# Performance work log

Measured on AMD Instinct MI355X. Metric: run time of the kernel, lower is better.

## Reference

```python
import jax, jax.numpy as jnp
import numpy as np

TD = 256  # text_dim


def conv1x1(x, w, b):
    # 1x1 conv == per-pixel matmul over channels; w: [out,in], x: [B,C,H,W]
    return jnp.einsum('oc,bchw->bohw', w, x) + b[None, :, None, None]


def setup_inputs() -> dict:
    key = jax.random.key(0)
    ks = iter(jax.random.split(key, 48))
    B = 4
    cin = [64, 128, 256, 512]
    vshapes = [(B, 64, 64, 64), (B, 128, 32, 32), (B, 256, 16, 16), (B, 512, 8, 8)]
    tshapes = [(B, TD, 64, 64), (B, TD, 32, 32), (B, TD, 16, 16), (B, TD, 8, 8)]
    d = {}
    for i, s in enumerate(vshapes):
        d[f'v{i}'] = jax.random.normal(next(ks), s, jnp.float32)
    for i, s in enumerate(tshapes):
        d[f't{i}'] = jax.random.normal(next(ks), s, jnp.float32)
    for i in range(4):
        d[f'vp_w{i}'] = jax.random.normal(next(ks), (TD, cin[i]), jnp.float32) / np.float32(np.sqrt(cin[i]))
        d[f'vp_b{i}'] = jnp.zeros((TD,), jnp.float32)
        d[f'op_w{i}'] = jax.random.normal(next(ks), (cin[i], TD), jnp.float32) / np.float32(np.sqrt(TD))
        d[f'op_b{i}'] = jnp.zeros((cin[i],), jnp.float32)
    for nm in ['q', 'k', 'v']:
        d[f'{nm}_w'] = jax.random.normal(next(ks), (TD, TD), jnp.float32) / np.float32(np.sqrt(TD))
        d[f'{nm}_b'] = jnp.zeros((TD,), jnp.float32)
    d['sg_w'] = jax.random.normal(next(ks), (TD, 4 * TD), jnp.float32) / np.float32(np.sqrt(4 * TD))
    d['sg_b'] = jnp.zeros((TD,), jnp.float32)
    d['bn_g'] = jnp.ones((TD,), jnp.float32)
    d['bn_b'] = jnp.zeros((TD,), jnp.float32)
    d['fc1_w'] = jax.random.normal(next(ks), (1024, TD), jnp.float32) / np.float32(np.sqrt(TD))
    d['fc1_b'] = jnp.zeros((1024,), jnp.float32)
    d['fc2_w'] = jax.random.normal(next(ks), (2048, 1024), jnp.float32) / np.float32(np.sqrt(1024))
    d['fc2_b'] = jnp.zeros((2048,), jnp.float32)
    return d


def reference(v0, v1, v2, v3, t0, t1, t2, t3,
              vp_w0, vp_b0, op_w0, op_b0,
              vp_w1, vp_b1, op_w1, op_b1,
              vp_w2, vp_b2, op_w2, op_b2,
              vp_w3, vp_b3, op_w3, op_b3,
              q_w, q_b, k_w, k_b, v_w, v_b,
              sg_w, sg_b, bn_g, bn_b, fc1_w, fc1_b, fc2_w, fc2_b):
    vs = [v0, v1, v2, v3]
    ts = [t0, t1, t2, t3]
    vpw = [vp_w0, vp_w1, vp_w2, vp_w3]
    vpb = [vp_b0, vp_b1, vp_b2, vp_b3]
    opw = [op_w0, op_w1, op_w2, op_w3]
    opb = [op_b0, op_b1, op_b2, op_b3]
    scale = np.float32(1.0 / np.sqrt(TD))

    enhanced = []
    for i in range(4):
        vp = conv1x1(vs[i], vpw[i], vpb[i])          # [B,TD,H,W]
        q = conv1x1(vp, q_w, q_b)
        k = conv1x1(ts[i], k_w, k_b)
        v = conv1x1(ts[i], v_w, v_b)
        B, C, H, W = vp.shape
        qf = q.reshape(B, C, H * W)                  # [B,C,Nq]
        kf = k.reshape(B, C, -1)                     # [B,C,Nk]
        vf = v.reshape(B, C, -1)                     # [B,C,Nk]
        attn = jax.nn.softmax(jnp.einsum('bcn,bcm->bnm', qf, kf) * scale, axis=-1)  # [B,Nq,Nk]
        av = jnp.einsum('bcm,bnm->bcn', vf, attn).reshape(B, C, H, W)
        enhanced.append(conv1x1(av, opw[i], opb[i]) + vs[i])

    # align text maps to smallest spatial size (divisible -> block average pool)
    s = ts[3].shape[2]
    pooled = [t.reshape(t.shape[0], t.shape[1], s, t.shape[2] // s, s, t.shape[3] // s).mean(axis=(3, 5))
              for t in ts]
    cat = jnp.concatenate(pooled, axis=1)            # [B,4*TD,s,s]
    x = conv1x1(cat, sg_w, sg_b)                     # [B,TD,s,s]
    # BatchNorm2d, training mode (batch statistics, biased variance)
    mu = x.mean(axis=(0, 2, 3), keepdims=True)
    var = x.var(axis=(0, 2, 3), keepdims=True)
    x = (x - mu) * jax.lax.rsqrt(var + 1e-5) * bn_g[None, :, None, None] + bn_b[None, :, None, None]
    x = jax.nn.relu(x).mean(axis=(2, 3))             # global avg pool -> [B,TD]
    x = jax.nn.relu(x @ fc1_w.T + fc1_b)
    x = x @ fc2_w.T + fc2_b                          # [B,2048]
    semantic = x.reshape(-1, 2, 1024)
    return (semantic, enhanced[0], enhanced[1], enhanced[2], enhanced[3])
```

## Files before the change

kernel.cpp:

```cpp
#include <hip/hip_runtime.h>

typedef __bf16 bf16_t;
typedef bf16_t bf16x8 __attribute__((ext_vector_type(8)));
typedef float f32x4 __attribute__((ext_vector_type(4)));
typedef unsigned short u16;
typedef unsigned long long u64;

__device__ __forceinline__ u16 f2bf(float f) {
  union { float f; unsigned u; } v; v.f = f;
  unsigned r = v.u + 0x7FFFu + ((v.u >> 16) & 1u);
  return (u16)(r >> 16);
}
__device__ __forceinline__ bf16x8 ld8(const u16* p) {
  return *reinterpret_cast<const bf16x8*>(p);
}
__device__ __forceinline__ void gload_lds16(const void* g, void* l) {
  __builtin_amdgcn_global_load_lds(
      (const __attribute__((address_space(1))) void*)g,
      (__attribute__((address_space(3))) void*)l, 16, 0, 0);
}

struct Ptrs4 { const float* p[4]; };

struct CvtJob { const float* s; u16* d; int n; };
struct CvtJobs { CvtJob j[8]; };

__global__ __launch_bounds__(256) void cvt_multi(CvtJobs jobs) {
  CvtJob J = jobs.j[blockIdx.y];
  for (int i = blockIdx.x * 256 + threadIdx.x; i < J.n; i += gridDim.x * 256)
    J.d[i] = f2bf(J.s[i]);
}

struct TJob { const float* s; u16* d; int C, N, nbx, nbz, off; };
struct TJobs { TJob j[12]; };

__global__ __launch_bounds__(256) void transpose_batch(TJobs J, int nj) {
  int bid = blockIdx.x, ji = 0;
#pragma unroll
  for (int k = 1; k < 12; ++k)
    if (k < nj && bid >= J.j[k].off) ji = k;
  TJob job = J.j[ji];
  int local = bid - job.off;
  int z = local % job.nbz;
  int l2 = local / job.nbz;
  int bx = l2 % job.nbx, by = l2 / job.nbx;
  __shared__ float t[32][33];
  int tx = threadIdx.x & 31, ty = threadIdx.x >> 5;
  int n0 = bx * 32, c0 = by * 32;
  long zi = (long)z * job.C * job.N, zo = (long)z * job.N * job.C;
#pragma unroll
  for (int i = 0; i < 4; ++i)
    t[ty + 8 * i][tx] = job.s[zi + (long)(c0 + ty + 8 * i) * job.N + n0 + tx];
  __syncthreads();
#pragma unroll
  for (int i = 0; i < 4; ++i)
    job.d[zo + (long)(n0 + ty + 8 * i) * job.C + c0 + tx] = f2bf(t[tx][ty + 8 * i]);
}

struct GJob {
  const u16 *A, *X;
  const float *bias, *bias2;
  void *o1, *o2;
  const float* res;
  int M, N, K, nbx, nbz, off, mode;
};
struct GJobs { GJob j[8]; };

__global__ __launch_bounds__(256) void gemm_batch(GJobs J, int nj) {
  int bid = blockIdx.x, ji = 0;
#pragma unroll
  for (int k = 1; k < 8; ++k)
    if (k < nj && bid >= J.j[k].off) ji = k;
  GJob job = J.j[ji];
  int local = bid - job.off;
  const int z = local % job.nbz;
  int l2 = local / job.nbz;
  const int n0 = (l2 % job.nbx) * 64, m0 = (l2 / job.nbx) * 64;
  const int M = job.M, N = job.N, K = job.K;
  const u16* __restrict__ A = job.A;
  const u16* __restrict__ X = job.X;

  __shared__ __attribute__((aligned(16))) u16 As[64][40];
  __shared__ __attribute__((aligned(16))) u16 Bs[64][40];
  const int tid = threadIdx.x;
  const long Xz = (long)z * N * K;
  const int arow = tid >> 2, acol = (tid & 3) * 8;
  const int w = tid >> 6, lane = tid & 63, g = lane >> 4, ln = lane & 15;
  const int wm = (w >> 1) * 32, wn = (w & 1) * 32;
  f32x4 zero = {0.f, 0.f, 0.f, 0.f};
  f32x4 acc[2][2];
#pragma unroll
  for (int i = 0; i < 2; ++i)
#pragma unroll
    for (int j = 0; j < 2; ++j) acc[i][j] = zero;

  for (int k0 = 0; k0 < K; k0 += 32) {
    int4 av = *reinterpret_cast<const int4*>(A + (long)(m0 + arow) * K + k0 + acol);
    int4 bv = *reinterpret_cast<const int4*>(X + Xz + (long)(n0 + arow) * K + k0 + acol);
    __syncthreads();
    *reinterpret_cast<int4*>(&As[arow][acol]) = av;
    *reinterpret_cast<int4*>(&Bs[arow][acol]) = bv;
    __syncthreads();
    bf16x8 a0 = ld8(&As[wm + ln][g * 8]);
    bf16x8 a1 = ld8(&As[wm + 16 + ln][g * 8]);
    bf16x8 b0 = ld8(&Bs[wn + ln][g * 8]);
    bf16x8 b1 = ld8(&Bs[wn + 16 + ln][g * 8]);
    acc[0][0] = __builtin_amdgcn_mfma_f32_16x16x32_bf16(a0, b0, acc[0][0], 0, 0, 0);
    acc[0][1] = __builtin_amdgcn_mfma_f32_16x16x32_bf16(a0, b1, acc[0][1], 0, 0, 0);
    acc[1][0] = __builtin_amdgcn_mfma_f32_16x16x32_bf16(a1, b0, acc[1][0], 0, 0, 0);
    acc[1][1] = __builtin_amdgcn_mfma_f32_16x16x32_bf16(a1, b1, acc[1][1], 0, 0, 0);
  }

#pragma unroll
  for (int i = 0; i < 2; ++i) {
#pragma unroll
    for (int j = 0; j < 2; ++j) {
      int mr0 = m0 + wm + 16 * i + g * 4;
      int nc = n0 + wn + 16 * j + ln;
      if (job.mode == 0) {
        u64 pk = 0;
#pragma unroll
        for (int r = 0; r < 4; ++r) {
          float val = acc[i][j][r] + (job.bias ? job.bias[mr0 + r] : 0.f);
          pk |= (u64)f2bf(val) << (16 * r);
        }
        *reinterpret_cast<u64*>((u16*)job.o1 + ((long)z * N + nc) * M + mr0) = pk;
      } else if (job.mode == 1) {
#pragma unroll
        for (int r = 0; r < 4; ++r) {
          float val = acc[i][j][r] + (job.bias ? job.bias[mr0 + r] : 0.f);
          ((u16*)job.o1)[((long)z * M + mr0 + r) * N + nc] = f2bf(val);
        }
      } else if (job.mode == 2) {
#pragma unroll
        for (int r = 0; r < 4; ++r) {
          long idx = ((long)z * M + mr0 + r) * N + nc;
          float val = acc[i][j][r] + job.bias[mr0 + r];
          if (job.res) val += job.res[idx];
          ((float*)job.o1)[idx] = val;
        }
      } else {
        long tbase = (long)z * N * 256 + (long)(nc >> 5) * 8192;
        if (mr0 < 256) {
          u64 pk = 0;
#pragma unroll
          for (int r = 0; r < 4; ++r)
            pk |= (u64)f2bf(acc[i][j][r] + job.bias[mr0 + r]) << (16 * r);
          int byteoff = ((nc & 31) * 512 + mr0 * 2) ^ ((nc & 7) << 4);
          *reinterpret_cast<u64*>((char*)job.o1 + tbase * 2 + byteoff) = pk;
        } else {
          int d0 = mr0 - 256;
#pragma unroll
          for (int r = 0; r < 4; ++r) {
            int d = d0 + r;
            int byteoff = (d * 64 + (nc & 31) * 2) ^ ((d & 7) << 4);
            *reinterpret_cast<u16*>((char*)job.o2 + tbase * 2 + byteoff) =
                f2bf(acc[i][j][r] + job.bias2[d]);
          }
        }
      }
    }
  }
}

struct AJob { const u16 *Q, *K, *V; u16* O; int N, off; };
struct AJobs { AJob j[4]; };

__global__ __launch_bounds__(256, 2) void attn_batch(AJobs J, int nj) {
  __shared__ __attribute__((aligned(16))) char stKV[2][2][16384];
  __shared__ __attribute__((aligned(16))) u16 Ps[4][16][40];
  int bid = blockIdx.x, ji = 0;
#pragma unroll
  for (int k = 1; k < 4; ++k)
    if (k < nj && bid >= J.j[k].off) ji = k;
  AJob job = J.j[ji];
  int local = bid - job.off;
  const int z = local & 3, bx = local >> 2;
  const int N = job.N;
  const int tid = threadIdx.x;
  const int w = tid >> 6, lane = tid & 63;
  const int g = lane >> 4, ln = lane & 15;
  const int qrow = bx * 64 + w * 16 + ln;
  const float scale = 0.0625f;
  const int nt = N >> 5;
  const long tb = (long)z * nt;

  bf16x8 qf[8];
  {
    const u16* qp = job.Q + ((long)z * N + qrow) * 256 + g * 8;
#pragma unroll
    for (int cc = 0; cc < 8; ++cc) qf[cc] = ld8(qp + cc * 32);
  }
  f32x4 zero = {0.f, 0.f, 0.f, 0.f};
  f32x4 oacc[16];
#pragma unroll
  for (int ct = 0; ct < 16; ++ct) oacc[ct] = zero;
  float mrow = -1e30f, lrow = 0.f;

  const char* gsrc = (const char*)(w < 2 ? job.K : job.V);
  auto stage_tile = [&](int buf, int t) {
    const char* gp = gsrc + (tb + t) * 16384 + (w & 1) * 8192 + lane * 16;
    char* lp = &stKV[buf][w >> 1][(w & 1) * 8192];
#pragma unroll
    for (int q = 0; q < 8; ++q) gload_lds16(gp + q * 1024, lp + q * 1024);
  };

  stage_tile(0, 0);
  asm volatile("s_waitcnt vmcnt(0)" ::: "memory");
  __syncthreads();

  const int swz = (ln & 7) << 4;
  for (int t = 0; t < nt; ++t) {
    const int buf = t & 1;
    if (t + 1 < nt) stage_tile(buf ^ 1, t + 1);
    const char* Kb = &stKV[buf][0][0];
    const char* Vb = &stKV[buf][1][0];

    f32x4 s0 = zero, s1 = zero;
#pragma unroll
    for (int cc = 0; cc < 8; ++cc) {
      bf16x8 k0 = *reinterpret_cast<const bf16x8*>(Kb + ((ln * 512 + cc * 64 + g * 16) ^ swz));
      bf16x8 k1 = *reinterpret_cast<const bf16x8*>(Kb + (((16 + ln) * 512 + cc * 64 + g * 16) ^ swz));
      s0 = __builtin_amdgcn_mfma_f32_16x16x32_bf16(k0, qf[cc], s0, 0, 0, 0);
      s1 = __builtin_amdgcn_mfma_f32_16x16x32_bf16(k1, qf[cc], s1, 0, 0, 0);
    }
    float x[8];
#pragma unroll
    for (int r = 0; r < 4; ++r) { x[r] = s0[r] * scale; x[4 + r] = s1[r] * scale; }
    float lm = fmaxf(fmaxf(fmaxf(x[0], x[1]), fmaxf(x[2], x[3])),
                     fmaxf(fmaxf(x[4], x[5]), fmaxf(x[6], x[7])));
    lm = fmaxf(lm, __shfl_xor(lm, 16));
    lm = fmaxf(lm, __shfl_xor(lm, 32));
    if (!__all(lm - mrow <= 8.0f)) {
      float nm = fmaxf(mrow, lm);
      float fac = __expf(mrow - nm);
      mrow = nm;
      lrow *= fac;
#pragma unroll
      for (int ct = 0; ct < 16; ++ct)
#pragma unroll
        for (int r = 0; r < 4; ++r) oacc[ct][r] *= fac;
    }
    float ps = 0.f;
#pragma unroll
    for (int j2 = 0; j2 < 8; ++j2) { x[j2] = __expf(x[j2] - mrow); ps += x[j2]; }
    ps += __shfl_xor(ps, 16);
    ps += __shfl_xor(ps, 32);
    lrow += ps;
    u64 plo = (u64)f2bf(x[0]) | ((u64)f2bf(x[1]) << 16) |
              ((u64)f2bf(x[2]) << 32) | ((u64)f2bf(x[3]) << 48);
    u64 phi = (u64)f2bf(x[4]) | ((u64)f2bf(x[5]) << 16) |
              ((u64)f2bf(x[6]) << 32) | ((u64)f2bf(x[7]) << 48);
    *reinterpret_cast<u64*>(&Ps[w][ln][g * 4]) = plo;
    *reinterpret_cast<u64*>(&Ps[w][ln][16 + g * 4]) = phi;
    asm volatile("s_waitcnt lgkmcnt(0)" ::: "memory");
    bf16x8 pa = ld8(&Ps[w][ln][g * 8]);
#pragma unroll
    for (int ct = 0; ct < 16; ++ct) {
      bf16x8 vv = *reinterpret_cast<const bf16x8*>(
          Vb + (((ct * 16 + ln) * 64 + g * 16) ^ swz));
      oacc[ct] = __builtin_amdgcn_mfma_f32_16x16x32_bf16(vv, pa, oacc[ct], 0, 0, 0);
    }
    asm volatile("s_waitcnt vmcnt(0)" ::: "memory");
    __syncthreads();
  }

  const float rl = 1.f / lrow;
  u16* Oz = job.O + ((long)z * N + qrow) * 256;
#pragma unroll
  for (int ct = 0; ct < 16; ++ct) {
    u64 pk = 0;
#pragma unroll
    for (int r = 0; r < 4; ++r) pk |= (u64)f2bf(oacc[ct][r] * rl) << (16 * r);
    *reinterpret_cast<u64*>(Oz + ct * 16 + g * 4) = pk;
  }
}

__global__ __launch_bounds__(256) void qeb_k(const float* __restrict__ qw,
                                             const float* __restrict__ qb, Ptrs4 vpb,
                                             float* __restrict__ qeb) {
  int o = threadIdx.x;
  int lvl = blockIdx.x;
  const float* vb = vpb.p[lvl];
  float acc = qb[o];
  for (int k = 0; k < 256; ++k) acc += qw[o * 256 + k] * vb[k];
  qeb[lvl * 256 + o] = acc;
}

__global__ __launch_bounds__(256) void pool_k(Ptrs4 ts, u16* __restrict__ poolT) {
  int gt = blockIdx.x * 256 + threadIdx.x;
  int ch = gt & 1023;
  int pix = (gt >> 10) & 63;
  int b = gt >> 16;
  int level = ch >> 8, c = ch & 255;
  int H = 64 >> level;
  int f = H >> 3;
  int py = pix >> 3, px = pix & 7;
  const float* src = ts.p[level] + (((long)b * 256 + c) * H + py * f) * H + px * f;
  float s = 0.f;
  for (int dy = 0; dy < f; ++dy)
    for (int dx = 0; dx < f; ++dx) s += src[dy * H + dx];
  poolT[gt] = f2bf(s / (float)(f * f));
}

__global__ __launch_bounds__(64) void bn_k(const float* __restrict__ x,
                                           const float* __restrict__ gw,
                                           const float* __restrict__ gb,
                                           float* __restrict__ xp) {
  int ch = blockIdx.x, t = threadIdx.x;
  float v[4], s = 0.f, sq = 0.f;
#pragma unroll
  for (int b = 0; b < 4; ++b) {
    v[b] = x[((long)b * 256 + ch) * 64 + t];
    s += v[b];
    sq += v[b] * v[b];
  }
#pragma unroll
  for (int off = 32; off; off >>= 1) {
    s += __shfl_xor(s, off);
    sq += __shfl_xor(sq, off);
  }
  float mu = s * (1.f / 256.f);
  float var = sq * (1.f / 256.f) - mu * mu;
  float rstd = rsqrtf(var + 1e-5f);
  float G = gw[ch], Bb = gb[ch];
#pragma unroll
  for (int b = 0; b < 4; ++b) {
    float y = fmaxf((v[b] - mu) * rstd * G + Bb, 0.f);
#pragma unroll
    for (int off = 32; off; off >>= 1) y += __shfl_xor(y, off);
    if (t == 0) xp[b * 256 + ch] = y * (1.f / 64.f);
  }
}

__global__ __launch_bounds__(256) void fc1_k(const float* __restrict__ xp,
                                             const float* __restrict__ w,
                                             const float* __restrict__ bias,
                                             float* __restrict__ o1) {
  int gt = blockIdx.x * 256 + threadIdx.x;
  int b = gt >> 10, j = gt & 1023;
  float acc = bias[j];
  const float* wr = w + (long)j * 256;
  const float* xr = xp + b * 256;
  for (int k = 0; k < 256; ++k) acc += xr[k] * wr[k];
  o1[gt] = fmaxf(acc, 0.f);
}

__global__ __launch_bounds__(256) void fc2_k(const float* __restrict__ o1,
                                             const float* __restrict__ w,
                                             const float* __restrict__ bias,
                                             float* __restrict__ out) {
  int gt = blockIdx.x * 256 + threadIdx.x;
  int b = gt >> 11, o = gt & 2047;
  float acc = bias[o];
  const float* wr = w + (long)o * 1024;
  const float* xr = o1 + b * 1024;
  for (int k = 0; k < 1024; ++k) acc += xr[k] * wr[k];
  out[gt] = acc;
}

extern "C" void kernel_launch(void* const* d_in, const int* in_sizes, int n_in,
                              void* d_out, int out_size, void* d_ws, size_t ws_size,
                              hipStream_t stream) {
  (void)in_sizes; (void)n_in; (void)out_size; (void)ws_size;
  const float *v_in[4], *t_in[4], *vp_w[4], *vp_b[4], *op_w[4], *op_b[4];
  for (int i = 0; i < 4; ++i) {
    v_in[i] = (const float*)d_in[i];
    t_in[i] = (const float*)d_in[4 + i];
    vp_w[i] = (const float*)d_in[8 + 4 * i];
    vp_b[i] = (const float*)d_in[9 + 4 * i];
    op_w[i] = (const float*)d_in[10 + 4 * i];
    op_b[i] = (const float*)d_in[11 + 4 * i];
  }
  const float* q_w = (const float*)d_in[24];
  const float* q_b = (const float*)d_in[25];
  const float* k_w = (const float*)d_in[26];
  const float* k_b = (const float*)d_in[27];
  const float* v_w = (const float*)d_in[28];
  const float* v_b = (const float*)d_in[29];
  const float* sg_w = (const float*)d_in[30];
  const float* sg_b = (const float*)d_in[31];
  const float* bn_g = (const float*)d_in[32];
  const float* bn_b = (const float*)d_in[33];
  const float* fc1_w = (const float*)d_in[34];
  const float* fc1_b = (const float*)d_in[35];
  const float* fc2_w = (const float*)d_in[36];
  const float* fc2_b = (const float*)d_in[37];
  float* out = (float*)d_out;

  const int cin[4] = {64, 128, 256, 512};
  const int NN[4] = {4096, 1024, 256, 64};
  const long NOFF[4] = {0, 4194304, 5242880, 5505024};
  const long VOFF[4] = {0, 1048576, 1572864, 1835008};

  char* ws = (char*)d_ws;
  size_t off = 0;
  auto alloc = [&](size_t bytes) {
    void* p = ws + off;
    off += (bytes + 255) & ~(size_t)255;
    return p;
  };
  u16* w_q = (u16*)alloc(65536 * 2);
  u16* w_kv = (u16*)alloc(131072 * 2);
  u16* w_op[4];
  for (int i = 0; i < 4; ++i) w_op[i] = (u16*)alloc((size_t)cin[i] * 256 * 2);
  u16* w_sg = (u16*)alloc(262144 * 2);
  u16* vpwT[4];
  for (int i = 0; i < 4; ++i) vpwT[i] = (u16*)alloc((size_t)cin[i] * 256 * 2);
  u16* qe[4];
  for (int i = 0; i < 4; ++i) qe[i] = (u16*)alloc((size_t)256 * cin[i] * 2);
  float* qeb = (float*)alloc(1024 * 4);
  u16* vT = (u16*)alloc((size_t)1966080 * 2);
  u16* tT = (u16*)alloc((size_t)5570560 * 2);
  u16* QT = (u16*)alloc((size_t)5570560 * 2);
  u16* Kt = (u16*)alloc((size_t)5570560 * 2);
  u16* Vt = (u16*)alloc((size_t)5570560 * 2);
  u16* Ob = (u16*)alloc((size_t)5570560 * 2);
  u16* poolT = (u16*)alloc((size_t)262144 * 2);
  float* xbuf = (float*)alloc((size_t)65536 * 4);
  float* xp = (float*)alloc(1024 * 4);
  float* fc1o = (float*)alloc(4096 * 4);

  CvtJobs jobs;
  jobs.j[0] = {q_w, w_q, 65536};
  jobs.j[1] = {k_w, w_kv, 65536};
  jobs.j[2] = {v_w, w_kv + 65536, 65536};
  jobs.j[3] = {op_w[0], w_op[0], cin[0] * 256};
  jobs.j[4] = {op_w[1], w_op[1], cin[1] * 256};
  jobs.j[5] = {op_w[2], w_op[2], cin[2] * 256};
  jobs.j[6] = {op_w[3], w_op[3], cin[3] * 256};
  jobs.j[7] = {sg_w, w_sg, 262144};
  cvt_multi<<<dim3(32, 8), 256, 0, stream>>>(jobs);

  {
    TJobs T;
    int boff = 0, nj = 0;
    for (int i = 0; i < 4; ++i) {
      int nbx = cin[i] / 32;
      T.j[nj] = {vp_w[i], vpwT[i], 256, cin[i], nbx, 1, boff};
      boff += nbx * 8;
      ++nj;
    }
    for (int i = 0; i < 4; ++i) {
      int nbx = NN[i] / 32, nby = cin[i] / 32;
      T.j[nj] = {v_in[i], vT + VOFF[i], cin[i], NN[i], nbx, 4, boff};
      boff += nbx * nby * 4;
      ++nj;
    }
    for (int i = 0; i < 4; ++i) {
      int nbx = NN[i] / 32;
      T.j[nj] = {t_in[i], tT + NOFF[i], 256, NN[i], nbx, 4, boff};
      boff += nbx * 8 * 4;
      ++nj;
    }
    transpose_batch<<<boff, 256, 0, stream>>>(T, nj);
  }

  {
    GJobs G;
    int boff = 0;
    for (int i = 0; i < 4; ++i) {
      int nbx = cin[i] / 64;
      G.j[i] = {w_q, vpwT[i], nullptr, nullptr, qe[i], nullptr, nullptr,
                256, cin[i], 256, nbx, 1, boff, 1};
      boff += nbx * 4;
    }
    gemm_batch<<<boff, 256, 0, stream>>>(G, 4);
  }
  Ptrs4 vpbp;
  for (int i = 0; i < 4; ++i) vpbp.p[i] = vp_b[i];
  qeb_k<<<4, 256, 0, stream>>>(q_w, q_b, vpbp, qeb);

  {
    GJobs G;
    int boff = 0, nj = 0;
    for (int i = 0; i < 4; ++i) {
      int nbx = NN[i] / 64;
      G.j[nj] = {qe[i], vT + VOFF[i], qeb + 256 * i, nullptr, QT + NOFF[i], nullptr,
                 nullptr, 256, NN[i], cin[i], nbx, 4, boff, 0};
      boff += nbx * 4 * 4;
      ++nj;
    }
    for (int i = 0; i < 4; ++i) {
      int nbx = NN[i] / 64;
      G.j[nj] = {w_kv, tT + NOFF[i], k_b, v_b, Kt + NOFF[i], Vt + NOFF[i], nullptr,
                 512, NN[i], 256, nbx, 4, boff, 3};
      boff += nbx * 8 * 4;
      ++nj;
    }
    gemm_batch<<<boff, 256, 0, stream>>>(G, 8);
  }

  {
    AJobs A;
    int boff = 0;
    for (int i = 0; i < 4; ++i) {
      A.j[i] = {QT + NOFF[i], Kt + NOFF[i], Vt + NOFF[i], Ob + NOFF[i], NN[i], boff};
      boff += (NN[i] / 64) * 4;
    }
    attn_batch<<<boff, 256, 0, stream>>>(A, 4);
  }

  Ptrs4 tp;
  for (int i = 0; i < 4; ++i) tp.p[i] = t_in[i];
  pool_k<<<1024, 256, 0, stream>>>(tp, poolT);

  const long enh_off[4] = {8192, 8192 + 1048576, 8192 + 1048576 + 524288,
                           8192 + 1048576 + 524288 + 262144};
  {
    GJobs G;
    int boff = 0;
    for (int i = 0; i < 4; ++i) {
      int nbx = NN[i] / 64, nby = cin[i] / 64;
      G.j[i] = {w_op[i], Ob + NOFF[i], op_b[i], nullptr, out + enh_off[i], nullptr,
                v_in[i], cin[i], NN[i], 256, nbx, 4, boff, 2};
      boff += nbx * nby * 4;
    }
    G.j[4] = {w_sg, poolT, sg_b, nullptr, xbuf, nullptr, nullptr,
              256, 64, 1024, 1, 4, boff, 2};
    boff += 1 * 4 * 4;
    gemm_batch<<<boff, 256, 0, stream>>>(G, 5);
  }

  bn_k<<<256, 64, 0, stream>>>(xbuf, bn_g, bn_b, xp);
  fc1_k<<<16, 256, 0, stream>>>(xp, fc1_w, fc1_b, fc1o);
  fc2_k<<<32, 256, 0, stream>>>(fc1o, fc2_w, fc2_b, out);
}
```

Baseline: 378.7 us.

## Process two query sub-tiles per wave in attention to reuse K/V fragments

The attention kernel drops from 4 waves to 2 waves per block, with each wave now handling 32 query rows as two 16-row halves. Each K and V fragment read from LDS feeds two MFMAs instead of one, which halves LDS read traffic per unit of compute. Block indices are also remapped so adjacent blocks share the same batch for K/V cache locality. In exchange the accumulators double to 128 floats per thread, raising register pressure and possibly occupancy loss. Each wave also now stages a full 16KB K or V tile per step instead of half of one.

```diff
diff --git a/kernel.cpp b/kernel.cpp
--- a/kernel.cpp
+++ b/kernel.cpp
@@ -166,43 +166,55 @@
 struct AJob { const u16 *Q, *K, *V; u16* O; int N, off; };
 struct AJobs { AJob j[4]; };
 
-__global__ __launch_bounds__(256, 2) void attn_batch(AJobs J, int nj) {
+__global__ __launch_bounds__(128, 2) void attn_batch(AJobs J, int nj) {
   __shared__ __attribute__((aligned(16))) char stKV[2][2][16384];
-  __shared__ __attribute__((aligned(16))) u16 Ps[4][16][40];
+  __shared__ __attribute__((aligned(16))) u16 Ps[2][32][40];
   int bid = blockIdx.x, ji = 0;
 #pragma unroll
   for (int k = 1; k < 4; ++k)
     if (k < nj && bid >= J.j[k].off) ji = k;
   AJob job = J.j[ji];
   int local = bid - job.off;
-  const int z = local & 3, bx = local >> 2;
   const int N = job.N;
+  const int nbx = N >> 6;
+  int z, bx;
+  if (nbx >= 2) {
+    z = (local & 7) >> 1;
+    bx = ((local >> 3) << 1) | (local & 1);
+  } else {
+    z = local & 3;
+    bx = 0;
+  }
   const int tid = threadIdx.x;
   const int w = tid >> 6, lane = tid & 63;
   const int g = lane >> 4, ln = lane & 15;
-  const int qrow = bx * 64 + w * 16 + ln;
   const float scale = 0.0625f;
   const int nt = N >> 5;
   const long tb = (long)z * nt;
-
-  bf16x8 qf[8];
-  {
-    const u16* qp = job.Q + ((long)z * N + qrow) * 256 + g * 8;
-#pragma unroll
-    for (int cc = 0; cc < 8; ++cc) qf[cc] = ld8(qp + cc * 32);
+  const int qbase = bx * 64 + w * 32;
+
+  bf16x8 qf[2][8];
+#pragma unroll
+  for (int qh = 0; qh < 2; ++qh) {
+    const u16* qp = job.Q + ((long)z * N + qbase + qh * 16 + ln) * 256 + g * 8;
+#pragma unroll
+    for (int cc = 0; cc < 8; ++cc) qf[qh][cc] = ld8(qp + cc * 32);
   }
   f32x4 zero = {0.f, 0.f, 0.f, 0.f};
-  f32x4 oacc[16];
-#pragma unroll
-  for (int ct = 0; ct < 16; ++ct) oacc[ct] = zero;
-  float mrow = -1e30f, lrow = 0.f;
-
-  const char* gsrc = (const char*)(w < 2 ? job.K : job.V);
+  f32x4 oacc[16][2];
+#pragma unroll
+  for (int ct = 0; ct < 16; ++ct) {
+    oacc[ct][0] = zero;
+    oacc[ct][1] = zero;
+  }
+  float mrow[2] = {-1e30f, -1e30f}, lrow[2] = {0.f, 0.f};
+
+  const char* gsrc = (const char*)(w ? job.V : job.K);
   auto stage_tile = [&](int buf, int t) {
-    const char* gp = gsrc + (tb + t) * 16384 + (w & 1) * 8192 + lane * 16;
-    char* lp = &stKV[buf][w >> 1][(w & 1) * 8192];
-#pragma unroll
-    for (int q = 0; q < 8; ++q) gload_lds16(gp + q * 1024, lp + q * 1024);
+    const char* gp = gsrc + (tb + t) * 16384 + lane * 16;
+    char* lp = &stKV[buf][w][0];
+#pragma unroll
+    for (int q = 0; q < 16; ++q) gload_lds16(gp + q * 1024, lp + q * 1024);
   };
 
   stage_tile(0, 0);
@@ -216,63 +228,74 @@
     const char* Kb = &stKV[buf][0][0];
     const char* Vb = &stKV[buf][1][0];
 
-    f32x4 s0 = zero, s1 = zero;
+    f32x4 s[2][2];
+    s[0][0] = zero; s[0][1] = zero; s[1][0] = zero; s[1][1] = zero;
 #pragma unroll
     for (int cc = 0; cc < 8; ++cc) {
       bf16x8 k0 = *reinterpret_cast<const bf16x8*>(Kb + ((ln * 512 + cc * 64 + g * 16) ^ swz));
       bf16x8 k1 = *reinterpret_cast<const bf16x8*>(Kb + (((16 + ln) * 512 + cc * 64 + g * 16) ^ swz));
-      s0 = __builtin_amdgcn_mfma_f32_16x16x32_bf16(k0, qf[cc], s0, 0, 0, 0);
-      s1 = __builtin_amdgcn_mfma_f32_16x16x32_bf16(k1, qf[cc], s1, 0, 0, 0);
-    }
-    float x[8];
-#pragma unroll
-    for (int r = 0; r < 4; ++r) { x[r] = s0[r] * scale; x[4 + r] = s1[r] * scale; }
-    float lm = fmaxf(fmaxf(fmaxf(x[0], x[1]), fmaxf(x[2], x[3])),
-                     fmaxf(fmaxf(x[4], x[5]), fmaxf(x[6], x[7])));
-    lm = fmaxf(lm, __shfl_xor(lm, 16));
-    lm = fmaxf(lm, __shfl_xor(lm, 32));
-    if (!__all(lm - mrow <= 8.0f)) {
-      float nm = fmaxf(mrow, lm);
-      float fac = __expf(mrow - nm);
-      mrow = nm;
-      lrow *= fac;
-#pragma unroll
-      for (int ct = 0; ct < 16; ++ct)
-#pragma unroll
-        for (int r = 0; r < 4; ++r) oacc[ct][r] *= fac;
-    }
-    float ps = 0.f;
-#pragma unroll
-    for (int j2 = 0; j2 < 8; ++j2) { x[j2] = __expf(x[j2] - mrow); ps += x[j2]; }
-    ps += __shfl_xor(ps, 16);
-    ps += __shfl_xor(ps, 32);
-    lrow += ps;
-    u64 plo = (u64)f2bf(x[0]) | ((u64)f2bf(x[1]) << 16) |
-              ((u64)f2bf(x[2]) << 32) | ((u64)f2bf(x[3]) << 48);
-    u64 phi = (u64)f2bf(x[4]) | ((u64)f2bf(x[5]) << 16) |
-              ((u64)f2bf(x[6]) << 32) | ((u64)f2bf(x[7]) << 48);
-    *reinterpret_cast<u64*>(&Ps[w][ln][g * 4]) = plo;
-    *reinterpret_cast<u64*>(&Ps[w][ln][16 + g * 4]) = phi;
+      s[0][0] = __builtin_amdgcn_mfma_f32_16x16x32_bf16(k0, qf[0][cc], s[0][0], 0, 0, 0);
+      s[0][1] = __builtin_amdgcn_mfma_f32_16x16x32_bf16(k0, qf[1][cc], s[0][1], 0, 0, 0);
+      s[1][0] = __builtin_amdgcn_mfma_f32_16x16x32_bf16(k1, qf[0][cc], s[1][0], 0, 0, 0);
+      s[1][1] = __builtin_amdgcn_mfma_f32_16x16x32_bf16(k1, qf[1][cc], s[1][1], 0, 0, 0);
+    }
+#pragma unroll
+    for (int qh = 0; qh < 2; ++qh) {
+      float x[8];
+#pragma unroll
+      for (int r = 0; r < 4; ++r) { x[r] = s[0][qh][r] * scale; x[4 + r] = s[1][qh][r] * scale; }
+      float lm = fmaxf(fmaxf(fmaxf(x[0], x[1]), fmaxf(x[2], x[3])),
+                       fmaxf(fmaxf(x[4], x[5]), fmaxf(x[6], x[7])));
+      lm = fmaxf(lm, __shfl_xor(lm, 16));
+      lm = fmaxf(lm, __shfl_xor(lm, 32));
+      if (!__all(lm - mrow[qh] <= 8.0f)) {
+        float nm = fmaxf(mrow[qh], lm);
+        float fac = __expf(mrow[qh] - nm);
+        mrow[qh] = nm;
+        lrow[qh] *= fac;
+#pragma unroll
+        for (int ct = 0; ct < 16; ++ct)
+#pragma unroll
+          for (int r = 0; r < 4; ++r) oacc[ct][qh][r] *= fac;
+      }
+      float ps = 0.f;
+#pragma unroll
+      for (int j2 = 0; j2 < 8; ++j2) { x[j2] = __expf(x[j2] - mrow[qh]); ps += x[j2]; }
+      ps += __shfl_xor(ps, 16);
+      ps += __shfl_xor(ps, 32);
+      lrow[qh] += ps;
+      u64 plo = (u64)f2bf(x[0]) | ((u64)f2bf(x[1]) << 16) |
+                ((u64)f2bf(x[2]) << 32) | ((u64)f2bf(x[3]) << 48);
+      u64 phi = (u64)f2bf(x[4]) | ((u64)f2bf(x[5]) << 16) |
+                ((u64)f2bf(x[6]) << 32) | ((u64)f2bf(x[7]) << 48);
+      *reinterpret_cast<u64*>(&Ps[w][qh * 16 + ln][g * 4]) = plo;
+      *reinterpret_cast<u64*>(&Ps[w][qh * 16 + ln][16 + g * 4]) = phi;
+    }
     asm volatile("s_waitcnt lgkmcnt(0)" ::: "memory");
-    bf16x8 pa = ld8(&Ps[w][ln][g * 8]);
+    bf16x8 pa0 = ld8(&Ps[w][ln][g * 8]);
+    bf16x8 pa1 = ld8(&Ps[w][16 + ln][g * 8]);
 #pragma unroll
     for (int ct = 0; ct < 16; ++ct) {
       bf16x8 vv = *reinterpret_cast<const bf16x8*>(
           Vb + (((ct * 16 + ln) * 64 + g * 16) ^ swz));
-      oacc[ct] = __builtin_amdgcn_mfma_f32_16x16x32_bf16(vv, pa, oacc[ct], 0, 0, 0);
+      oacc[ct][0] = __builtin_amdgcn_mfma_f32_16x16x32_bf16(vv, pa0, oacc[ct][0], 0, 0, 0);
+      oacc[ct][1] = __builtin_amdgcn_mfma_f32_16x16x32_bf16(vv, pa1, oacc[ct][1], 0, 0, 0);
     }
     asm volatile("s_waitcnt vmcnt(0)" ::: "memory");
     __syncthreads();
   }
 
-  const float rl = 1.f / lrow;
-  u16* Oz = job.O + ((long)z * N + qrow) * 256;
-#pragma unroll
-  for (int ct = 0; ct < 16; ++ct) {
-    u64 pk = 0;
-#pragma unroll
-    for (int r = 0; r < 4; ++r) pk |= (u64)f2bf(oacc[ct][r] * rl) << (16 * r);
-    *reinterpret_cast<u64*>(Oz + ct * 16 + g * 4) = pk;
+#pragma unroll
+  for (int qh = 0; qh < 2; ++qh) {
+    const float rl = 1.f / lrow[qh];
+    u16* Oz = job.O + ((long)z * N + qbase + qh * 16 + ln) * 256;
+#pragma unroll
+    for (int ct = 0; ct < 16; ++ct) {
+      u64 pk = 0;
+#pragma unroll
+      for (int r = 0; r < 4; ++r) pk |= (u64)f2bf(oacc[ct][qh][r] * rl) << (16 * r);
+      *reinterpret_cast<u64*>(Oz + ct * 16 + g * 4) = pk;
+    }
   }
 }
 
@@ -498,7 +521,7 @@
       A.j[i] = {QT + NOFF[i], Kt + NOFF[i], Vt + NOFF[i], Ob + NOFF[i], NN[i], boff};
       boff += (NN[i] / 64) * 4;
     }
-    attn_batch<<<boff, 256, 0, stream>>>(A, 4);
+    attn_batch<<<boff, 128, 0, stream>>>(A, 4);
   }
 
   Ptrs4 tp;
```

After: 468.1 us. 23.6% more time.
